# Kernel tuning notes

Hardware: AMD Instinct MI355X
Metric: run time of the kernel (lower is better)

## Reference

```python
import jax, jax.numpy as jnp
import numpy as np

HIDDEN = 128

def setup_inputs() -> dict:
    key = jax.random.key(0)
    k1, k2, k3, k4, k5, k6 = jax.random.split(key, 6)
    n_nodes, n_edges, h = 100000, 500000, HIDDEN
    node_features_after_gcn = jax.random.normal(k1, (n_nodes, h), dtype=jnp.float32)
    edges = jax.random.randint(k2, (2, n_edges), 0, n_nodes, dtype=jnp.int64)
    # edge_classifier params: Linear(2h -> 4h), Linear(4h -> 2)
    W1 = jax.random.normal(k3, (2 * h, 4 * h), dtype=jnp.float32) / np.sqrt(2 * h)
    b1 = jax.random.normal(k4, (4 * h,), dtype=jnp.float32) * 0.01
    W2 = jax.random.normal(k5, (4 * h, 2), dtype=jnp.float32) / np.sqrt(4 * h)
    b2 = jax.random.normal(k6, (2,), dtype=jnp.float32) * 0.01
    return {"node_features_after_gcn": node_features_after_gcn, "edges": edges,
            "W1": W1, "b1": b1, "W2": W2, "b2": b2}

def reference(node_features_after_gcn, W1, b1, W2, b2, edges):
    # gather endpoint features: [E, h] each (node1/node2 projections are Identity)
    first = node_features_after_gcn[edges[0], :]
    second = node_features_after_gcn[edges[1], :]
    edge_feat = jnp.concatenate((first, second), axis=1)  # [E, 2h]
    edge_feat = jax.nn.relu(edge_feat)
    hidden = jax.nn.relu(edge_feat @ W1 + b1)  # [E, 4h]
    return hidden @ W2 + b2  # [E, 2]
```

## Files before the change

### kernel.cpp

```cpp
#include <hip/hip_runtime.h>
#include <stdint.h>

#define HID  128
#define N1   512
#define NCAT 1024
#define NTB  48

typedef _Float16 f16;
typedef __attribute__((ext_vector_type(8))) _Float16 f16x8;
typedef __attribute__((ext_vector_type(4))) _Float16 f16x4;
typedef __attribute__((ext_vector_type(8))) short   short8;
typedef __attribute__((ext_vector_type(4))) float   floatx4;
typedef __attribute__((ext_vector_type(2))) float   floatx2;
typedef __attribute__((ext_vector_type(8))) __bf16  bf16x8;

static __device__ __forceinline__ short f2bf(float x) {
  uint32_t u = __builtin_bit_cast(uint32_t, x);
  uint32_t r = (u + 0x7FFFu + ((u >> 16) & 1u)) >> 16;
  return (short)r;
}
static __device__ __forceinline__ float bf2f(short s) {
  uint32_t u = ((uint32_t)(uint16_t)s) << 16;
  return __builtin_bit_cast(float, u);
}

static __device__ __forceinline__ void gload16(const f16* g, f16* l) {
  __builtin_amdgcn_global_load_lds(
      (const __attribute__((address_space(1))) unsigned int*)g,
      (__attribute__((address_space(3))) unsigned int*)l, 16, 0, 0);
}


__global__ __launch_bounds__(256) void prep_all(
    const float* __restrict__ feats, const float* __restrict__ W1,
    f16* __restrict__ A, f16* __restrict__ BT2, int total4) {
  int idx = blockIdx.x * 256 + threadIdx.x;
  if (idx < total4) {
    floatx4 f = *(const floatx4*)(feats + (size_t)idx * 4);
    f16x4 o;
#pragma unroll
    for (int j = 0; j < 4; ++j) o[j] = (f16)fmaxf(f[j], 0.f);
    *(f16x4*)(A + (size_t)idx * 4) = o;
    return;
  }
  int w = idx - total4;
  if (w < N1 * 256) {
    int n = w >> 8;
    int k = w & 255;
    BT2[w] = (f16)W1[k * N1 + n];
  }
}

__global__ __launch_bounds__(512, 2) void fused_kernel(
    const f16* __restrict__ A,
    const f16* __restrict__ BT2,
    const float* __restrict__ b1,
    const float* __restrict__ W2,
    const float* __restrict__ b2,
    const int* __restrict__ edges,
    float* __restrict__ out,
    int n_edges, int ntiles) {
  __shared__ f16 AU[2][NTB][HID];
  __shared__ f16 AV[2][NTB][HID];
  __shared__ float   part[8][NTB][2];
  __shared__ float   b1s[N1];
  __shared__ floatx2 w2s[N1];

  const int tid  = threadIdx.x;
  const int wave = tid >> 6;
  const int lane = tid & 63;
  const int quad = lane >> 4;
  const int l16  = lane & 15;
  const int n0w  = wave << 6;

  if (tid < N1) {
    b1s[tid] = b1[tid];
    w2s[tid] = *(const floatx2*)(W2 + 2 * tid);
  }

  f16x8 bfr[4][8];
#pragma unroll
  for (int nn = 0; nn < 4; ++nn) {
    const f16* bp = BT2 + (size_t)(n0w + nn * 16 + l16) * 256 + quad * 8;
#pragma unroll
    for (int kk = 0; kk < 8; ++kk) bfr[nn][kk] = *(const f16x8*)(bp + kk * 32);
  }

  const int j0   = wave * 3;
  const int rsub = lane >> 4;

  int idr[3];
  auto load_idx = [&](int t) {
#pragma unroll
    for (int c = 0; c < 3; ++c) {
      int j = j0 + c;
      int side = (j >= 12) ? 1 : 0;
      int r = ((j - side * 12) << 2) + rsub;
      int e = t * NTB + r;
      if (e >= n_edges) e = n_edges - 1;
      idr[c] = edges[side * n_edges + e];
    }
  };
  auto issue_gather = [&](int bb) {
#pragma unroll
    for (int c = 0; c < 3; ++c) {
      int j = j0 + c;
      int side = (j >= 12) ? 1 : 0;
      int r0 = (j - side * 12) << 2;
      int r  = r0 + rsub;
      const f16* src = A + ((size_t)idr[c] << 7) + (((lane & 15) ^ (r & 15)) << 3);
      f16* dst = side ? &AV[bb][r0][0] : &AU[bb][r0][0];
      gload16(src, dst);
    }
  };

  const int NB = gridDim.x;
  const int t0 = blockIdx.x;
  if (t0 < ntiles) {
    load_idx(t0);
    issue_gather(0);
    load_idx(t0 + NB);
  }

  int bb = 0;
  for (int t = t0; t < ntiles; t += NB) {
    __syncthreads();

    if (t + NB < ntiles) {
      issue_gather(bb ^ 1);
      load_idx(t + 2 * NB);
    }

    floatx4 acc[3][4];
#pragma unroll
    for (int mt = 0; mt < 3; ++mt)
#pragma unroll
      for (int nn = 0; nn < 4; ++nn) acc[mt][nn] = (floatx4){0.f, 0.f, 0.f, 0.f};

    const f16* au = &AU[bb][0][0];
    const f16* av = &AV[bb][0][0];
#pragma unroll
    for (int kk = 0; kk < 8; ++kk) {
      const f16* base = (kk < 4) ? au : av;
      const int coff = (((((kk & 3) << 2) + quad)) ^ l16) << 3;
      f16x8 a0 = *(const f16x8*)(base + (0 * 16 + l16) * HID + coff);
      f16x8 a1 = *(const f16x8*)(base + (1 * 16 + l16) * HID + coff);
      f16x8 a2 = *(const f16x8*)(base + (2 * 16 + l16) * HID + coff);
#pragma unroll
      for (int nn = 0; nn < 4; ++nn) {
        acc[0][nn] = __builtin_amdgcn_mfma_f32_16x16x32_f16(bfr[nn][kk], a0, acc[0][nn], 0, 0, 0);
        acc[1][nn] = __builtin_amdgcn_mfma_f32_16x16x32_f16(bfr[nn][kk], a1, acc[1][nn], 0, 0, 0);
        acc[2][nn] = __builtin_amdgcn_mfma_f32_16x16x32_f16(bfr[nn][kk], a2, acc[2][nn], 0, 0, 0);
      }
    }

    float s0[3] = {0.f, 0.f, 0.f};
    float s1[3] = {0.f, 0.f, 0.f};
#pragma unroll
    for (int nn = 0; nn < 4; ++nn) {
      const int nb = n0w + nn * 16 + (quad << 2);
      const floatx4 bv = *(const floatx4*)&b1s[nb];
      const floatx2 wa = w2s[nb + 0];
      const floatx2 wb = w2s[nb + 1];
      const floatx2 wc = w2s[nb + 2];
      const floatx2 wd = w2s[nb + 3];
#pragma unroll
      for (int mt = 0; mt < 3; ++mt) {
        float p0 = fmaxf(acc[mt][nn][0] + bv[0], 0.f);
        float p1 = fmaxf(acc[mt][nn][1] + bv[1], 0.f);
        float p2 = fmaxf(acc[mt][nn][2] + bv[2], 0.f);
        float p3 = fmaxf(acc[mt][nn][3] + bv[3], 0.f);
        s0[mt] += p0 * wa[0] + p1 * wb[0] + p2 * wc[0] + p3 * wd[0];
        s1[mt] += p0 * wa[1] + p1 * wb[1] + p2 * wc[1] + p3 * wd[1];
      }
    }
#pragma unroll
    for (int mt = 0; mt < 3; ++mt) {
      float a0 = s0[mt] + __shfl_xor(s0[mt], 16);
      a0 += __shfl_xor(a0, 32);
      float a1 = s1[mt] + __shfl_xor(s1[mt], 16);
      a1 += __shfl_xor(a1, 32);
      if (quad == 0) {
        floatx2 o = {a0, a1};
        *(floatx2*)&part[wave][mt * 16 + l16][0] = o;
      }
    }
    __syncthreads();
    if (tid < 2 * NTB) {
      const int m  = tid >> 1;
      const int jj = tid & 1;
      float s = part[0][m][jj] + part[1][m][jj] + part[2][m][jj] + part[3][m][jj]
              + part[4][m][jj] + part[5][m][jj] + part[6][m][jj] + part[7][m][jj];
      const int e = t * NTB + m;
      if (e < n_edges) out[2 * (size_t)e + jj] = s + b2[jj];
    }
    bb ^= 1;
  }
}


__global__ __launch_bounds__(256) void conv_bt_bf(
    const float* __restrict__ W1, short* __restrict__ BT) {
  int idx = blockIdx.x * 256 + threadIdx.x;
  int n = idx >> 7;
  int k = idx & 127;
  float w = (n < N1) ? W1[k * N1 + n] : W1[(k + HID) * N1 + (n - N1)];
  BT[idx] = f2bf(w);
}

__global__ __launch_bounds__(256) void gemm_bf(
    const float* __restrict__ feats, const short* __restrict__ BT,
    short* __restrict__ GH, int n_nodes) {
  const int wave = threadIdx.x >> 6;
  const int lane = threadIdx.x & 63;
  const int quad = lane >> 4;
  const int l16  = lane & 15;
  const int row0 = blockIdx.x * 64 + wave * 16;
  const int n0   = blockIdx.y * 128;
  const int m  = row0 + l16;
  const int mc = (m < n_nodes) ? m : (n_nodes - 1);
  const float* arow = feats + (size_t)mc * HID;
  floatx4 acc[8];
#pragma unroll
  for (int i = 0; i < 8; ++i) acc[i] = (floatx4){0.f, 0.f, 0.f, 0.f};
#pragma unroll
  for (int kk = 0; kk < 4; ++kk) {
    const int kbase = kk * 32 + quad * 8;
    floatx4 a0 = *(const floatx4*)(arow + kbase);
    floatx4 a1 = *(const floatx4*)(arow + kbase + 4);
    short8 af;
#pragma unroll
    for (int j = 0; j < 4; ++j) { float x = a0[j]; af[j] = f2bf(x > 0.f ? x : 0.f); }
#pragma unroll
    for (int j = 0; j < 4; ++j) { float x = a1[j]; af[4 + j] = f2bf(x > 0.f ? x : 0.f); }
    bf16x8 afrag = __builtin_bit_cast(bf16x8, af);
#pragma unroll
    for (int nn = 0; nn < 8; ++nn) {
      const int n = n0 + nn * 16 + l16;
      short8 bs = *(const short8*)(BT + (size_t)n * HID + kbase);
      acc[nn] = __builtin_amdgcn_mfma_f32_16x16x32_bf16(
          afrag, __builtin_bit_cast(bf16x8, bs), acc[nn], 0, 0, 0);
    }
  }
#pragma unroll
  for (int nn = 0; nn < 8; ++nn) {
    const int col = n0 + nn * 16 + l16;
#pragma unroll
    for (int r = 0; r < 4; ++r) {
      const int row = row0 + quad * 4 + r;
      if (row < n_nodes) GH[(size_t)row * NCAT + col] = f2bf(acc[nn][r]);
    }
  }
}

__global__ __launch_bounds__(256) void edge2_bf(
    const short* __restrict__ GH, const int* __restrict__ edges,
    const float* __restrict__ b1, const float* __restrict__ W2,
    const float* __restrict__ b2, float* __restrict__ out, int n_edges) {
  const int wave = threadIdx.x >> 6;
  const int lane = threadIdx.x & 63;
  const int w = blockIdx.x * 4 + wave;
  const int e0 = 2 * w;
  if (e0 >= n_edges) return;
  const bool has1 = (e0 + 1 < n_edges);
  const int j0 = lane * 8;
  const int u0 = edges[e0];
  const int v0 = edges[n_edges + e0];
  const int u1 = has1 ? edges[e0 + 1] : u0;
  const int v1 = has1 ? edges[n_edges + e0 + 1] : v0;
  short8 g0 = *(const short8*)(GH + (size_t)u0 * NCAT + j0);
  short8 h0 = *(const short8*)(GH + (size_t)v0 * NCAT + N1 + j0);
  short8 g1 = *(const short8*)(GH + (size_t)u1 * NCAT + j0);
  short8 h1 = *(const short8*)(GH + (size_t)v1 * NCAT + N1 + j0);
  float bv[8];
  {
    floatx4 t0 = *(const floatx4*)(b1 + j0);
    floatx4 t1 = *(const floatx4*)(b1 + j0 + 4);
#pragma unroll
    for (int j = 0; j < 4; ++j) { bv[j] = t0[j]; bv[4 + j] = t1[j]; }
  }
  float wv[16];
#pragma unroll
  for (int q = 0; q < 4; ++q) {
    floatx4 tt = *(const floatx4*)(W2 + (size_t)j0 * 2 + q * 4);
#pragma unroll
    for (int j = 0; j < 4; ++j) wv[q * 4 + j] = tt[j];
  }
  float s00 = 0.f, s01 = 0.f, s10 = 0.f, s11 = 0.f;
#pragma unroll
  for (int j = 0; j < 8; ++j) {
    float p0 = bf2f(g0[j]) + bf2f(h0[j]) + bv[j];
    p0 = p0 > 0.f ? p0 : 0.f;
    s00 += p0 * wv[2 * j];
    s01 += p0 * wv[2 * j + 1];
    float p1 = bf2f(g1[j]) + bf2f(h1[j]) + bv[j];
    p1 = p1 > 0.f ? p1 : 0.f;
    s10 += p1 * wv[2 * j];
    s11 += p1 * wv[2 * j + 1];
  }
#pragma unroll
  for (int off = 32; off > 0; off >>= 1) {
    s00 += __shfl_down(s00, off, 64);
    s01 += __shfl_down(s01, off, 64);
    s10 += __shfl_down(s10, off, 64);
    s11 += __shfl_down(s11, off, 64);
  }
  if (lane == 0) {
    out[2 * (size_t)e0]     = s00 + b2[0];
    out[2 * (size_t)e0 + 1] = s01 + b2[1];
    if (has1) {
      out[2 * (size_t)e0 + 2] = s10 + b2[0];
      out[2 * (size_t)e0 + 3] = s11 + b2[1];
    }
  }
}

__global__ __launch_bounds__(256) void slow_kernel(
    const float* __restrict__ feats, const int* __restrict__ edges,
    const float* __restrict__ W1, const float* __restrict__ b1,
    const float* __restrict__ W2, const float* __restrict__ b2,
    float* __restrict__ out, int n_edges) {
  const int wave = threadIdx.x >> 6;
  const int lane = threadIdx.x & 63;
  const int edge = blockIdx.x * 4 + wave;
  if (edge >= n_edges) return;
  const int u = edges[edge];
  const int v = edges[n_edges + edge];
  float f[4];
  f[0] = feats[(size_t)u * HID + lane];
  f[1] = feats[(size_t)u * HID + 64 + lane];
  f[2] = feats[(size_t)v * HID + lane];
  f[3] = feats[(size_t)v * HID + 64 + lane];
#pragma unroll
  for (int i = 0; i < 4; ++i) f[i] = f[i] > 0.f ? f[i] : 0.f;
  const int j0 = lane * 8;
  float acc[8];
#pragma unroll
  for (int j = 0; j < 8; ++j) acc[j] = 0.f;
#pragma unroll
  for (int seg = 0; seg < 4; ++seg) {
    float fs = f[seg];
    for (int k2 = 0; k2 < 64; ++k2) {
      float fk = __shfl(fs, k2, 64);
      const float* wr = W1 + (size_t)(seg * 64 + k2) * N1 + j0;
#pragma unroll
      for (int j = 0; j < 8; ++j) acc[j] += fk * wr[j];
    }
  }
  float s0 = 0.f, s1 = 0.f;
#pragma unroll
  for (int j = 0; j < 8; ++j) {
    float p = acc[j] + b1[j0 + j];
    p = p > 0.f ? p : 0.f;
    s0 += p * W2[(size_t)(j0 + j) * 2];
    s1 += p * W2[(size_t)(j0 + j) * 2 + 1];
  }
#pragma unroll
  for (int off = 32; off > 0; off >>= 1) {
    s0 += __shfl_down(s0, off, 64);
    s1 += __shfl_down(s1, off, 64);
  }
  if (lane == 0) {
    out[2 * (size_t)edge]     = s0 + b2[0];
    out[2 * (size_t)edge + 1] = s1 + b2[1];
  }
}

extern "C" void kernel_launch(void* const* d_in, const int* in_sizes, int n_in,
                              void* d_out, int out_size, void* d_ws, size_t ws_size,
                              hipStream_t stream) {
  const float* feats = (const float*)d_in[0];
  const int*   edges = (const int*)d_in[1];
  const float* W1    = (const float*)d_in[2];
  const float* b1    = (const float*)d_in[3];
  const float* W2    = (const float*)d_in[4];
  const float* b2    = (const float*)d_in[5];
  float* out = (float*)d_out;

  const int n_nodes = in_sizes[0] / HID;
  const int n_edges = in_sizes[1] / 2;

  const size_t bt2_bytes = (size_t)N1 * 256 * 2;
  const size_t a_bytes   = (size_t)n_nodes * HID * 2;

  const size_t bt_bytes = (size_t)NCAT * HID * 2;
  const size_t gh_bytes = (size_t)n_nodes * NCAT * 2;

  if (ws_size >= bt2_bytes + a_bytes) {
    f16* BT2 = (f16*)d_ws;
    f16* A   = (f16*)((char*)d_ws + bt2_bytes);
    const int total4 = n_nodes * (HID / 4);
    const int prep_total = total4 + N1 * 256;
    prep_all<<<(prep_total + 255) / 256, 256, 0, stream>>>(feats, W1, A, BT2, total4);
    const int ntiles = (n_edges + NTB - 1) / NTB;
    const int nb = ntiles < 256 ? ntiles : 256;
    fused_kernel<<<nb, 512, 0, stream>>>(A, BT2, b1, W2, b2, edges, out, n_edges, ntiles);
  } else if (ws_size >= bt_bytes + gh_bytes) {
    short* BT = (short*)d_ws;
    short* GH = (short*)((char*)d_ws + bt_bytes);
    conv_bt_bf<<<(NCAT * HID) / 256, 256, 0, stream>>>(W1, BT);
    dim3 grid((n_nodes + 63) / 64, NCAT / 128);
    gemm_bf<<<grid, 256, 0, stream>>>(feats, BT, GH, n_nodes);
    edge2_bf<<<((n_edges + 1) / 2 + 3) / 4, 256, 0, stream>>>(GH, edges, b1, W2, b2, out, n_edges);
  } else {
    slow_kernel<<<(n_edges + 3) / 4, 256, 0, stream>>>(feats, edges, W1, b1, W2, b2, out, n_edges);
  }
}
```

Measured before the change: 224.0 us.

## Double edge tile per block and use packed fp16 dot for second layer

Raises the per-block edge tile from 48 to 96 rows, processed as two 48-row MFMA passes per tile, so each sync and gather round covers twice as many edges. The second-layer epilogue converts the ReLU activations to packed fp16 and accumulates with fdot2 against W2 stored as fp16 pairs, replacing scalar fp32 FMAs. The larger tile doubles LDS use for the gather buffers, which may lower occupancy, and fp16 rounding of activations and W2 reduces precision.

```diff
diff --git a/kernel.cpp b/kernel.cpp
--- a/kernel.cpp
+++ b/kernel.cpp
@@ -4,11 +4,12 @@
 #define HID  128
 #define N1   512
 #define NCAT 1024
-#define NTB  48
+#define NTB  96
 
 typedef _Float16 f16;
 typedef __attribute__((ext_vector_type(8))) _Float16 f16x8;
 typedef __attribute__((ext_vector_type(4))) _Float16 f16x4;
+typedef __attribute__((ext_vector_type(2))) _Float16 f16x2;
 typedef __attribute__((ext_vector_type(8))) short   short8;
 typedef __attribute__((ext_vector_type(4))) float   floatx4;
 typedef __attribute__((ext_vector_type(2))) float   floatx2;
@@ -22,6 +23,18 @@
 static __device__ __forceinline__ float bf2f(short s) {
   uint32_t u = ((uint32_t)(uint16_t)s) << 16;
   return __builtin_bit_cast(float, u);
+}
+static __device__ __forceinline__ f16x2 pkrtz(float a, float b) {
+  return __builtin_bit_cast(f16x2, __builtin_amdgcn_cvt_pkrtz(a, b));
+}
+typedef __fp16 __attribute__((ext_vector_type(2))) fp16v2;
+static __device__ __forceinline__ float fdot2(f16x2 a, f16x2 b, float c) {
+#if __has_builtin(__builtin_amdgcn_fdot2)
+  return __builtin_amdgcn_fdot2(__builtin_bit_cast(fp16v2, a),
+                                __builtin_bit_cast(fp16v2, b), c, false);
+#else
+  return c + (float)a[0] * (float)b[0] + (float)a[1] * (float)b[1];
+#endif
 }
 
 static __device__ __forceinline__ void gload16(const f16* g, f16* l) {
@@ -62,9 +75,10 @@
     int n_edges, int ntiles) {
   __shared__ f16 AU[2][NTB][HID];
   __shared__ f16 AV[2][NTB][HID];
-  __shared__ float   part[8][NTB][2];
-  __shared__ float   b1s[N1];
-  __shared__ floatx2 w2s[N1];
+  __shared__ float part[8][NTB][2];
+  __shared__ float b1s[N1];
+  __shared__ f16x2 w2h0[N1 / 2];
+  __shared__ f16x2 w2h1[N1 / 2];
 
   const int tid  = threadIdx.x;
   const int wave = tid >> 6;
@@ -73,10 +87,13 @@
   const int l16  = lane & 15;
   const int n0w  = wave << 6;
 
-  if (tid < N1) {
-    b1s[tid] = b1[tid];
-    w2s[tid] = *(const floatx2*)(W2 + 2 * tid);
-  }
+  if (tid < N1) b1s[tid] = b1[tid];
+  if (tid < N1 / 2) {
+    floatx4 w = *(const floatx4*)(W2 + 4 * tid);
+    w2h0[tid] = pkrtz(w[0], w[2]);
+    w2h1[tid] = pkrtz(w[1], w[3]);
+  }
+  const float b2v0 = b2[0], b2v1 = b2[1];
 
   f16x8 bfr[4][8];
 #pragma unroll
@@ -86,30 +103,30 @@
     for (int kk = 0; kk < 8; ++kk) bfr[nn][kk] = *(const f16x8*)(bp + kk * 32);
   }
 
-  const int j0   = wave * 3;
+  const int j0   = wave * 6;
   const int rsub = lane >> 4;
 
-  int idr[3];
+  int idr[6];
   auto load_idx = [&](int t) {
 #pragma unroll
-    for (int c = 0; c < 3; ++c) {
+    for (int c = 0; c < 6; ++c) {
       int j = j0 + c;
-      int side = (j >= 12) ? 1 : 0;
-      int r = ((j - side * 12) << 2) + rsub;
+      int side = (j >= 24) ? 1 : 0;
+      int r = ((j - side * 24) << 2) + rsub;
       int e = t * NTB + r;
       if (e >= n_edges) e = n_edges - 1;
       idr[c] = edges[side * n_edges + e];
     }
   };
-  auto issue_gather = [&](int bb) {
-#pragma unroll
-    for (int c = 0; c < 3; ++c) {
+  auto issue_gather = [&](int b) {
+#pragma unroll
+    for (int c = 0; c < 6; ++c) {
       int j = j0 + c;
-      int side = (j >= 12) ? 1 : 0;
-      int r0 = (j - side * 12) << 2;
+      int side = (j >= 24) ? 1 : 0;
+      int r0 = (j - side * 24) << 2;
       int r  = r0 + rsub;
-      const f16* src = A + ((size_t)idr[c] << 7) + (((lane & 15) ^ (r & 15)) << 3);
-      f16* dst = side ? &AV[bb][r0][0] : &AU[bb][r0][0];
+      const f16* src = A + ((size_t)idr[c] << 7) + ((l16 ^ (r & 15)) << 3);
+      f16* dst = side ? &AV[b][r0][0] : &AU[b][r0][0];
       gload16(src, dst);
     }
   };
@@ -131,60 +148,66 @@
       load_idx(t + 2 * NB);
     }
 
-    floatx4 acc[3][4];
-#pragma unroll
-    for (int mt = 0; mt < 3; ++mt)
-#pragma unroll
-      for (int nn = 0; nn < 4; ++nn) acc[mt][nn] = (floatx4){0.f, 0.f, 0.f, 0.f};
-
     const f16* au = &AU[bb][0][0];
     const f16* av = &AV[bb][0][0];
-#pragma unroll
-    for (int kk = 0; kk < 8; ++kk) {
-      const f16* base = (kk < 4) ? au : av;
-      const int coff = (((((kk & 3) << 2) + quad)) ^ l16) << 3;
-      f16x8 a0 = *(const f16x8*)(base + (0 * 16 + l16) * HID + coff);
-      f16x8 a1 = *(const f16x8*)(base + (1 * 16 + l16) * HID + coff);
-      f16x8 a2 = *(const f16x8*)(base + (2 * 16 + l16) * HID + coff);
+
+#pragma unroll
+    for (int pass = 0; pass < 2; ++pass) {
+      const int rbase = pass * 48;
+      floatx4 acc[3][4];
+#pragma unroll
+      for (int mt = 0; mt < 3; ++mt)
+#pragma unroll
+        for (int nn = 0; nn < 4; ++nn) acc[mt][nn] = (floatx4){0.f, 0.f, 0.f, 0.f};
+
+#pragma unroll
+      for (int kk = 0; kk < 8; ++kk) {
+        const f16* base = (kk < 4) ? au : av;
+        const int coff = (((((kk & 3) << 2) + quad)) ^ l16) << 3;
+        f16x8 a0 = *(const f16x8*)(base + (rbase + 0 * 16 + l16) * HID + coff);
+        f16x8 a1 = *(const f16x8*)(base + (rbase + 1 * 16 + l16) * HID + coff);
+        f16x8 a2 = *(const f16x8*)(base + (rbase + 2 * 16 + l16) * HID + coff);
+#pragma unroll
+        for (int nn = 0; nn < 4; ++nn) {
+          acc[0][nn] = __builtin_amdgcn_mfma_f32_16x16x32_f16(bfr[nn][kk], a0, acc[0][nn], 0, 0, 0);
+          acc[1][nn] = __builtin_amdgcn_mfma_f32_16x16x32_f16(bfr[nn][kk], a1, acc[1][nn], 0, 0, 0);
+          acc[2][nn] = __builtin_amdgcn_mfma_f32_16x16x32_f16(bfr[nn][kk], a2, acc[2][nn], 0, 0, 0);
+        }
+      }
+
+      float s0[3] = {0.f, 0.f, 0.f};
+      float s1[3] = {0.f, 0.f, 0.f};
 #pragma unroll
       for (int nn = 0; nn < 4; ++nn) {
-        acc[0][nn] = __builtin_amdgcn_mfma_f32_16x16x32_f16(bfr[nn][kk], a0, acc[0][nn], 0, 0, 0);
-        acc[1][nn] = __builtin_amdgcn_mfma_f32_16x16x32_f16(bfr[nn][kk], a1, acc[1][nn], 0, 0, 0);
-        acc[2][nn] = __builtin_amdgcn_mfma_f32_16x16x32_f16(bfr[nn][kk], a2, acc[2][nn], 0, 0, 0);
+        const int nb = n0w + nn * 16 + (quad << 2);
+        const floatx4 bv  = *(const floatx4*)&b1s[nb];
+        const f16x4 wq0 = *(const f16x4*)&w2h0[nb >> 1];
+        const f16x4 wq1 = *(const f16x4*)&w2h1[nb >> 1];
+#pragma unroll
+        for (int mt = 0; mt < 3; ++mt) {
+          floatx2 a01 = {acc[mt][nn][0] + bv[0], acc[mt][nn][1] + bv[1]};
+          floatx2 a23 = {acc[mt][nn][2] + bv[2], acc[mt][nn][3] + bv[3]};
+          a01 = __builtin_elementwise_max(a01, (floatx2){0.f, 0.f});
+          a23 = __builtin_elementwise_max(a23, (floatx2){0.f, 0.f});
+          f16x2 z01 = pkrtz(a01[0], a01[1]);
+          f16x2 z23 = pkrtz(a23[0], a23[1]);
+          s0[mt] = fdot2(z01, (f16x2){wq0[0], wq0[1]}, s0[mt]);
+          s0[mt] = fdot2(z23, (f16x2){wq0[2], wq0[3]}, s0[mt]);
+          s1[mt] = fdot2(z01, (f16x2){wq1[0], wq1[1]}, s1[mt]);
+          s1[mt] = fdot2(z23, (f16x2){wq1[2], wq1[3]}, s1[mt]);
+        }
       }
-    }
-
-    float s0[3] = {0.f, 0.f, 0.f};
-    float s1[3] = {0.f, 0.f, 0.f};
-#pragma unroll
-    for (int nn = 0; nn < 4; ++nn) {
-      const int nb = n0w + nn * 16 + (quad << 2);
-      const floatx4 bv = *(const floatx4*)&b1s[nb];
-      const floatx2 wa = w2s[nb + 0];
-      const floatx2 wb = w2s[nb + 1];
-      const floatx2 wc = w2s[nb + 2];
-      const floatx2 wd = w2s[nb + 3];
 #pragma unroll
       for (int mt = 0; mt < 3; ++mt) {
-        float p0 = fmaxf(acc[mt][nn][0] + bv[0], 0.f);
-        float p1 = fmaxf(acc[mt][nn][1] + bv[1], 0.f);
-        float p2 = fmaxf(acc[mt][nn][2] + bv[2], 0.f);
-        float p3 = fmaxf(acc[mt][nn][3] + bv[3], 0.f);
-        s0[mt] += p0 * wa[0] + p1 * wb[0] + p2 * wc[0] + p3 * wd[0];
-        s1[mt] += p0 * wa[1] + p1 * wb[1] + p2 * wc[1] + p3 * wd[1];
+        float a0 = s0[mt] + __shfl_xor(s0[mt], 16);
+        a0 += __shfl_xor(a0, 32);
+        float a1 = s1[mt] + __shfl_xor(s1[mt], 16);
+        a1 += __shfl_xor(a1, 32);
+        if (quad == 0)
+          *(floatx2*)&part[wave][rbase + mt * 16 + l16][0] = (floatx2){a0, a1};
       }
     }
-#pragma unroll
-    for (int mt = 0; mt < 3; ++mt) {
-      float a0 = s0[mt] + __shfl_xor(s0[mt], 16);
-      a0 += __shfl_xor(a0, 32);
-      float a1 = s1[mt] + __shfl_xor(s1[mt], 16);
-      a1 += __shfl_xor(a1, 32);
-      if (quad == 0) {
-        floatx2 o = {a0, a1};
-        *(floatx2*)&part[wave][mt * 16 + l16][0] = o;
-      }
-    }
+
     __syncthreads();
     if (tid < 2 * NTB) {
       const int m  = tid >> 1;
@@ -192,7 +215,7 @@
       float s = part[0][m][jj] + part[1][m][jj] + part[2][m][jj] + part[3][m][jj]
               + part[4][m][jj] + part[5][m][jj] + part[6][m][jj] + part[7][m][jj];
       const int e = t * NTB + m;
-      if (e < n_edges) out[2 * (size_t)e + jj] = s + b2[jj];
+      if (e < n_edges) out[2 * (size_t)e + jj] = s + (jj ? b2v1 : b2v0);
     }
     bb ^= 1;
   }
```

Result: slower. 251.7 us (+12.4%).
